# Performance work log

Measured on AMD Instinct MI355X. Metric: run time of the kernel, lower is better.

The kernel has to match this reference:

```python
import jax, jax.numpy as jnp
import numpy as np

N_NODES = 100000
D_FEAT = 128
N_EDGES = 300000
HIDDEN = 64


def setup_inputs() -> dict:
    key = jax.random.key(0)
    k1, k2, k3, k4 = jax.random.split(key, 4)
    node_emb = jax.random.normal(k1, (N_NODES, D_FEAT), dtype=jnp.float32)
    train_sample = jax.random.randint(k2, (N_EDGES, 2), 0, N_NODES, dtype=jnp.int64)
    input_dim = 2 * D_FEAT
    r1 = np.sqrt(6.0 / input_dim)
    w1 = jax.random.uniform(k3, (input_dim, HIDDEN), minval=-r1, maxval=r1, dtype=jnp.float32)
    b1 = jnp.zeros((HIDDEN,), dtype=jnp.float32)
    r2 = np.sqrt(6.0 / HIDDEN)
    w2 = jax.random.uniform(k4, (HIDDEN, 1), minval=-r2, maxval=r2, dtype=jnp.float32)
    return {"input": node_emb, "train_sample": train_sample, "w1": w1, "b1": b1, "w2": w2}


def reference(input, train_sample, w1, b1, w2):
    # gather source/target node embeddings: [E, D] each
    src = input[train_sample[:, 0]]
    dst = input[train_sample[:, 1]]
    h = jnp.concatenate([src, dst], axis=1)  # [E, 2D]
    x = jax.nn.relu(h @ w1 + b1)             # [E, HIDDEN]
    return x @ w2                             # [E, 1]
```

## Files before the change

kernel.cpp:

```cpp
#include <hip/hip_runtime.h>
#include <hip/hip_bf16.h>


#define D_FEAT 128
#define HIDDEN 64

typedef __attribute__((ext_vector_type(8))) short v8s;
typedef __attribute__((ext_vector_type(4))) float f32x4;

__device__ inline unsigned short f2bf(float f) {
    unsigned u = __builtin_bit_cast(unsigned, f);
    unsigned r = (u + 0x7FFFu + ((u >> 16) & 1u)) >> 16;
    return (unsigned short)r;
}
__device__ inline float bf2f(unsigned short u) {
    return __builtin_bit_cast(float, (unsigned)u << 16);
}

__device__ inline bool detect_is64(const int* ts32, int lane) {
    int probe = ts32[2 * lane + 1];
    return __ballot(probe != 0) == 0ULL;
}

__global__ void __launch_bounds__(256)
precompute_kernel(const float* __restrict__ emb, const float* __restrict__ w1,
                  const float* __restrict__ b1, unsigned short* __restrict__ P,
                  int n_nodes) {
    __shared__ unsigned short bt[16384];
    const int t = threadIdx.x;

    {
        const int k    = t & 127;
        const int half = t >> 7;
        const float4* src = reinterpret_cast<const float4*>(w1 + (size_t)t * 64);
#pragma unroll
        for (int j4 = 0; j4 < 16; ++j4) {
            const float4 v = src[j4];
            const int cb = half * 64 + j4 * 4;
            bt[((cb + 0) * 128 + k) ^ (((cb + 0) & 7) << 3)] = f2bf(v.x);
            bt[((cb + 1) * 128 + k) ^ (((cb + 1) & 7) << 3)] = f2bf(v.y);
            bt[((cb + 2) * 128 + k) ^ (((cb + 2) & 7) << 3)] = f2bf(v.z);
            bt[((cb + 3) * 128 + k) ^ (((cb + 3) & 7) << 3)] = f2bf(v.w);
        }
    }
    __syncthreads();

    const int lane = t & 63;
    const int wid  = t >> 6;
    const int sub  = lane & 15;
    const int g    = lane >> 4;
    const int base = blockIdx.x * 128 + wid * 32;

    const float* aptr[2];
#pragma unroll
    for (int tl = 0; tl < 2; ++tl) {
        int arow = base + tl * 16 + sub;
        if (arow >= n_nodes) arow = n_nodes - 1;
        aptr[tl] = emb + (size_t)arow * D_FEAT + g * 8;
    }

    f32x4 acc[2][8];
#pragma unroll
    for (int tl = 0; tl < 2; ++tl)
#pragma unroll
        for (int nj = 0; nj < 8; ++nj) acc[tl][nj] = (f32x4){0.f, 0.f, 0.f, 0.f};

#pragma unroll
    for (int ks = 0; ks < 4; ++ks) {
        const int k0 = ks * 32;
        v8s af[2];
#pragma unroll
        for (int tl = 0; tl < 2; ++tl) {
            const float4 a0 = *reinterpret_cast<const float4*>(aptr[tl] + k0);
            const float4 a1 = *reinterpret_cast<const float4*>(aptr[tl] + k0 + 4);
            af[tl][0] = (short)f2bf(a0.x); af[tl][1] = (short)f2bf(a0.y);
            af[tl][2] = (short)f2bf(a0.z); af[tl][3] = (short)f2bf(a0.w);
            af[tl][4] = (short)f2bf(a1.x); af[tl][5] = (short)f2bf(a1.y);
            af[tl][6] = (short)f2bf(a1.z); af[tl][7] = (short)f2bf(a1.w);
        }
#pragma unroll
        for (int nj = 0; nj < 8; ++nj) {
            const int c = nj * 16 + sub;
            const int eidx = (c * 128 + k0 + g * 8) ^ ((c & 7) << 3);
            const v8s bf = *reinterpret_cast<const v8s*>(&bt[eidx]);
            acc[0][nj] = __builtin_amdgcn_mfma_f32_16x16x32_bf16(bf, af[0], acc[0][nj], 0, 0, 0);
            acc[1][nj] = __builtin_amdgcn_mfma_f32_16x16x32_bf16(bf, af[1], acc[1][nj], 0, 0, 0);
        }
    }

    float4 bias[4];
#pragma unroll
    for (int nj = 0; nj < 4; ++nj)
        bias[nj] = *reinterpret_cast<const float4*>(b1 + nj * 16 + g * 4);

#pragma unroll
    for (int tl = 0; tl < 2; ++tl) {
        const int node = base + tl * 16 + sub;
        if (node < n_nodes) {
#pragma unroll
            for (int nj = 0; nj < 8; ++nj) {
                float b0 = 0.f, b1v = 0.f, b2 = 0.f, b3 = 0.f;
                if (nj < 4) { b0 = bias[nj].x; b1v = bias[nj].y;
                              b2 = bias[nj].z; b3 = bias[nj].w; }
                ushort4 o;
                o.x = f2bf(acc[tl][nj][0] + b0);
                o.y = f2bf(acc[tl][nj][1] + b1v);
                o.z = f2bf(acc[tl][nj][2] + b2);
                o.w = f2bf(acc[tl][nj][3] + b3);
                *reinterpret_cast<ushort4*>(P + (size_t)node * 128 + nj * 16 + g * 4) = o;
            }
        }
    }
}

__global__ void __launch_bounds__(256)
edge_kernel(const unsigned short* __restrict__ P, const void* __restrict__ ts,
            const float* __restrict__ w2, float* __restrict__ out, int n_edges) {
    const int lane = threadIdx.x & 63;
    const int wid  = threadIdx.x >> 6;
    const int sub  = lane & 15;
    const int grp  = lane >> 4;
    const int gw   = blockIdx.x * 4 + wid;
    const int nw   = gridDim.x * 4;

    const int* ts32 = (const int*)ts;
    const long long* ts64 = (const long long*)ts;
    const bool is64 = detect_is64(ts32, lane);

    const float4 w2v = *reinterpret_cast<const float4*>(w2 + sub * 4);

    for (int e = gw * 4 + grp; e < n_edges; e += nw * 4) {
        long long s, d;
        if (is64) { s = ts64[2 * e]; d = ts64[2 * e + 1]; }
        else      { s = ts32[2 * e]; d = ts32[2 * e + 1]; }
        const ushort4 a = *reinterpret_cast<const ushort4*>(P + (size_t)s * 128 + sub * 4);
        const ushort4 b = *reinterpret_cast<const ushort4*>(P + (size_t)d * 128 + 64 + sub * 4);
        float h0 = bf2f(a.x) + bf2f(b.x);
        float h1 = bf2f(a.y) + bf2f(b.y);
        float h2 = bf2f(a.z) + bf2f(b.z);
        float h3 = bf2f(a.w) + bf2f(b.w);
        h0 = h0 > 0.f ? h0 : 0.f; h1 = h1 > 0.f ? h1 : 0.f;
        h2 = h2 > 0.f ? h2 : 0.f; h3 = h3 > 0.f ? h3 : 0.f;
        float v = h0 * w2v.x + h1 * w2v.y + h2 * w2v.z + h3 * w2v.w;
#pragma unroll
        for (int off = 8; off > 0; off >>= 1) v += __shfl_xor(v, off);
        if (sub == 0) out[e] = v;
    }
}

__global__ void __launch_bounds__(256)
direct_kernel(const float* __restrict__ emb, const void* __restrict__ ts,
              const float* __restrict__ w1, const float* __restrict__ b1,
              const float* __restrict__ w2, float* __restrict__ out, int n_edges) {
    const int lane = threadIdx.x & 63;
    const int gw   = blockIdx.x * (blockDim.x >> 6) + (threadIdx.x >> 6);
    const int nw   = gridDim.x * (blockDim.x >> 6);
    const float w2v  = w2[lane];
    const float bias = b1[lane];
    const int* ts32 = (const int*)ts;
    const long long* ts64 = (const long long*)ts;
    const bool is64 = detect_is64(ts32, lane);

    for (int e = gw; e < n_edges; e += nw) {
        long long s, d;
        if (is64) { s = ts64[2 * e]; d = ts64[2 * e + 1]; }
        else      { s = ts32[2 * e]; d = ts32[2 * e + 1]; }
        const float4* s4 = reinterpret_cast<const float4*>(emb + s * D_FEAT);
        const float4* d4 = reinterpret_cast<const float4*>(emb + d * D_FEAT);
        float acc = bias;
#pragma unroll
        for (int k4 = 0; k4 < 32; ++k4) {
            float4 r = s4[k4];
            acc += r.x * w1[(4 * k4 + 0) * 64 + lane];
            acc += r.y * w1[(4 * k4 + 1) * 64 + lane];
            acc += r.z * w1[(4 * k4 + 2) * 64 + lane];
            acc += r.w * w1[(4 * k4 + 3) * 64 + lane];
        }
#pragma unroll
        for (int k4 = 0; k4 < 32; ++k4) {
            float4 r = d4[k4];
            acc += r.x * w1[(128 + 4 * k4 + 0) * 64 + lane];
            acc += r.y * w1[(128 + 4 * k4 + 1) * 64 + lane];
            acc += r.z * w1[(128 + 4 * k4 + 2) * 64 + lane];
            acc += r.w * w1[(128 + 4 * k4 + 3) * 64 + lane];
        }
        float h = acc > 0.0f ? acc : 0.0f;
        float v = h * w2v;
#pragma unroll
        for (int off = 32; off > 0; off >>= 1) v += __shfl_xor(v, off);
        if (lane == 0) out[e] = v;
    }
}

extern "C" void kernel_launch(void* const* d_in, const int* in_sizes, int n_in,
                              void* d_out, int out_size, void* d_ws, size_t ws_size,
                              hipStream_t stream) {
    const float* emb = (const float*)d_in[0];
    const void*  ts  = d_in[1];
    const float* w1  = (const float*)d_in[2];
    const float* b1  = (const float*)d_in[3];
    const float* w2  = (const float*)d_in[4];
    float* out = (float*)d_out;

    const int n_nodes = in_sizes[0] / D_FEAT;
    const int n_edges = in_sizes[1] / 2;

    const size_t p_bytes = (size_t)n_nodes * 128 * sizeof(unsigned short);

    if (ws_size >= p_bytes) {
        unsigned short* P = (unsigned short*)d_ws;
        const int nblocks = (n_nodes + 127) / 128;
        precompute_kernel<<<nblocks, 256, 0, stream>>>(emb, w1, b1, P, n_nodes);
        edge_kernel<<<2048, 256, 0, stream>>>(P, ts, w2, out, n_edges);
    } else {
        direct_kernel<<<2048, 256, 0, stream>>>(emb, ts, w1, b1, w2, out, n_edges);
    }
}
```

Before: 45.68 us.

## Shrink precompute tile, prefetch A before LDS fill, widen edge loads

The precompute kernel now gives each wave 16 nodes instead of 32 and launches twice as many blocks with a min-blocks launch bound, so the MFMA stage uses fewer registers and more blocks can be resident. The embedding rows are loaded into registers before the W1 shared-memory fill, so that global load latency overlaps the LDS writes. The edge kernel uses 8 lanes per edge with 16-byte loads instead of 16 lanes with 8-byte loads, which halves the shuffle reduction depth and doubles the edges handled per wave. The cost is that every block still stages the full W1 tile into LDS, and there are now twice as many blocks doing so.

Measured after the change: 45.89 us. No clear change (+0.5%).

```diff
diff --git a/kernel.cpp b/kernel.cpp
--- a/kernel.cpp
+++ b/kernel.cpp
@@ -22,12 +22,27 @@
     return __ballot(probe != 0) == 0ULL;
 }
 
-__global__ void __launch_bounds__(256)
+__global__ void __launch_bounds__(256, 4)
 precompute_kernel(const float* __restrict__ emb, const float* __restrict__ w1,
                   const float* __restrict__ b1, unsigned short* __restrict__ P,
                   int n_nodes) {
     __shared__ unsigned short bt[16384];
-    const int t = threadIdx.x;
+    const int t    = threadIdx.x;
+    const int lane = t & 63;
+    const int wid  = t >> 6;
+    const int sub  = lane & 15;
+    const int g    = lane >> 4;
+    const int m0   = blockIdx.x * 64 + wid * 16;
+
+    int arow = m0 + sub;
+    if (arow >= n_nodes) arow = n_nodes - 1;
+    const float* aptr = emb + (size_t)arow * D_FEAT + g * 8;
+    float4 a[8];
+#pragma unroll
+    for (int ks = 0; ks < 4; ++ks) {
+        a[2 * ks]     = *reinterpret_cast<const float4*>(aptr + ks * 32);
+        a[2 * ks + 1] = *reinterpret_cast<const float4*>(aptr + ks * 32 + 4);
+    }
 
     {
         const int k    = t & 127;
@@ -45,46 +60,25 @@
     }
     __syncthreads();
 
-    const int lane = t & 63;
-    const int wid  = t >> 6;
-    const int sub  = lane & 15;
-    const int g    = lane >> 4;
-    const int base = blockIdx.x * 128 + wid * 32;
-
-    const float* aptr[2];
-#pragma unroll
-    for (int tl = 0; tl < 2; ++tl) {
-        int arow = base + tl * 16 + sub;
-        if (arow >= n_nodes) arow = n_nodes - 1;
-        aptr[tl] = emb + (size_t)arow * D_FEAT + g * 8;
-    }
-
-    f32x4 acc[2][8];
-#pragma unroll
-    for (int tl = 0; tl < 2; ++tl)
-#pragma unroll
-        for (int nj = 0; nj < 8; ++nj) acc[tl][nj] = (f32x4){0.f, 0.f, 0.f, 0.f};
+    f32x4 acc[8];
+#pragma unroll
+    for (int nj = 0; nj < 8; ++nj) acc[nj] = (f32x4){0.f, 0.f, 0.f, 0.f};
 
 #pragma unroll
     for (int ks = 0; ks < 4; ++ks) {
         const int k0 = ks * 32;
-        v8s af[2];
-#pragma unroll
-        for (int tl = 0; tl < 2; ++tl) {
-            const float4 a0 = *reinterpret_cast<const float4*>(aptr[tl] + k0);
-            const float4 a1 = *reinterpret_cast<const float4*>(aptr[tl] + k0 + 4);
-            af[tl][0] = (short)f2bf(a0.x); af[tl][1] = (short)f2bf(a0.y);
-            af[tl][2] = (short)f2bf(a0.z); af[tl][3] = (short)f2bf(a0.w);
-            af[tl][4] = (short)f2bf(a1.x); af[tl][5] = (short)f2bf(a1.y);
-            af[tl][6] = (short)f2bf(a1.z); af[tl][7] = (short)f2bf(a1.w);
-        }
+        const float4 a0 = a[2 * ks], a1 = a[2 * ks + 1];
+        v8s af;
+        af[0] = (short)f2bf(a0.x); af[1] = (short)f2bf(a0.y);
+        af[2] = (short)f2bf(a0.z); af[3] = (short)f2bf(a0.w);
+        af[4] = (short)f2bf(a1.x); af[5] = (short)f2bf(a1.y);
+        af[6] = (short)f2bf(a1.z); af[7] = (short)f2bf(a1.w);
 #pragma unroll
         for (int nj = 0; nj < 8; ++nj) {
             const int c = nj * 16 + sub;
             const int eidx = (c * 128 + k0 + g * 8) ^ ((c & 7) << 3);
             const v8s bf = *reinterpret_cast<const v8s*>(&bt[eidx]);
-            acc[0][nj] = __builtin_amdgcn_mfma_f32_16x16x32_bf16(bf, af[0], acc[0][nj], 0, 0, 0);
-            acc[1][nj] = __builtin_amdgcn_mfma_f32_16x16x32_bf16(bf, af[1], acc[1][nj], 0, 0, 0);
+            acc[nj] = __builtin_amdgcn_mfma_f32_16x16x32_bf16(bf, af, acc[nj], 0, 0, 0);
         }
     }
 
@@ -93,24 +87,31 @@
     for (int nj = 0; nj < 4; ++nj)
         bias[nj] = *reinterpret_cast<const float4*>(b1 + nj * 16 + g * 4);
 
-#pragma unroll
-    for (int tl = 0; tl < 2; ++tl) {
-        const int node = base + tl * 16 + sub;
-        if (node < n_nodes) {
-#pragma unroll
-            for (int nj = 0; nj < 8; ++nj) {
-                float b0 = 0.f, b1v = 0.f, b2 = 0.f, b3 = 0.f;
-                if (nj < 4) { b0 = bias[nj].x; b1v = bias[nj].y;
-                              b2 = bias[nj].z; b3 = bias[nj].w; }
-                ushort4 o;
-                o.x = f2bf(acc[tl][nj][0] + b0);
-                o.y = f2bf(acc[tl][nj][1] + b1v);
-                o.z = f2bf(acc[tl][nj][2] + b2);
-                o.w = f2bf(acc[tl][nj][3] + b3);
-                *reinterpret_cast<ushort4*>(P + (size_t)node * 128 + nj * 16 + g * 4) = o;
-            }
-        }
-    }
+    const int node = m0 + sub;
+    if (node < n_nodes) {
+#pragma unroll
+        for (int nj = 0; nj < 8; ++nj) {
+            float b0 = 0.f, b1v = 0.f, b2 = 0.f, b3 = 0.f;
+            if (nj < 4) { b0 = bias[nj].x; b1v = bias[nj].y;
+                          b2 = bias[nj].z; b3 = bias[nj].w; }
+            ushort4 o;
+            o.x = f2bf(acc[nj][0] + b0);
+            o.y = f2bf(acc[nj][1] + b1v);
+            o.z = f2bf(acc[nj][2] + b2);
+            o.w = f2bf(acc[nj][3] + b3);
+            *reinterpret_cast<ushort4*>(P + (size_t)node * 128 + nj * 16 + g * 4) = o;
+        }
+    }
+}
+
+__device__ inline float pairterm(unsigned aw, unsigned bw, float w0, float w1) {
+    float a0 = __builtin_bit_cast(float, aw << 16);
+    float a1 = __builtin_bit_cast(float, aw & 0xFFFF0000u);
+    float b0 = __builtin_bit_cast(float, bw << 16);
+    float b1 = __builtin_bit_cast(float, bw & 0xFFFF0000u);
+    float h0 = a0 + b0; h0 = h0 > 0.f ? h0 : 0.f;
+    float h1 = a1 + b1; h1 = h1 > 0.f ? h1 : 0.f;
+    return h0 * w0 + h1 * w1;
 }
 
 __global__ void __launch_bounds__(256)
@@ -118,8 +119,8 @@
             const float* __restrict__ w2, float* __restrict__ out, int n_edges) {
     const int lane = threadIdx.x & 63;
     const int wid  = threadIdx.x >> 6;
-    const int sub  = lane & 15;
-    const int grp  = lane >> 4;
+    const int sub  = lane & 7;
+    const int grp  = lane >> 3;
     const int gw   = blockIdx.x * 4 + wid;
     const int nw   = gridDim.x * 4;
 
@@ -127,23 +128,21 @@
     const long long* ts64 = (const long long*)ts;
     const bool is64 = detect_is64(ts32, lane);
 
-    const float4 w2v = *reinterpret_cast<const float4*>(w2 + sub * 4);
-
-    for (int e = gw * 4 + grp; e < n_edges; e += nw * 4) {
+    const float4 w2a = *reinterpret_cast<const float4*>(w2 + sub * 8);
+    const float4 w2b = *reinterpret_cast<const float4*>(w2 + sub * 8 + 4);
+
+    for (int e = gw * 8 + grp; e < n_edges; e += nw * 8) {
         long long s, d;
         if (is64) { s = ts64[2 * e]; d = ts64[2 * e + 1]; }
         else      { s = ts32[2 * e]; d = ts32[2 * e + 1]; }
-        const ushort4 a = *reinterpret_cast<const ushort4*>(P + (size_t)s * 128 + sub * 4);
-        const ushort4 b = *reinterpret_cast<const ushort4*>(P + (size_t)d * 128 + 64 + sub * 4);
-        float h0 = bf2f(a.x) + bf2f(b.x);
-        float h1 = bf2f(a.y) + bf2f(b.y);
-        float h2 = bf2f(a.z) + bf2f(b.z);
-        float h3 = bf2f(a.w) + bf2f(b.w);
-        h0 = h0 > 0.f ? h0 : 0.f; h1 = h1 > 0.f ? h1 : 0.f;
-        h2 = h2 > 0.f ? h2 : 0.f; h3 = h3 > 0.f ? h3 : 0.f;
-        float v = h0 * w2v.x + h1 * w2v.y + h2 * w2v.z + h3 * w2v.w;
-#pragma unroll
-        for (int off = 8; off > 0; off >>= 1) v += __shfl_xor(v, off);
+        const uint4 a = *reinterpret_cast<const uint4*>(P + (size_t)s * 128 + sub * 8);
+        const uint4 b = *reinterpret_cast<const uint4*>(P + (size_t)d * 128 + 64 + sub * 8);
+        float v = pairterm(a.x, b.x, w2a.x, w2a.y)
+                + pairterm(a.y, b.y, w2a.z, w2a.w)
+                + pairterm(a.z, b.z, w2b.x, w2b.y)
+                + pairterm(a.w, b.w, w2b.z, w2b.w);
+#pragma unroll
+        for (int off = 1; off < 8; off <<= 1) v += __shfl_xor(v, off);
         if (sub == 0) out[e] = v;
     }
 }
@@ -209,7 +208,7 @@
 
     if (ws_size >= p_bytes) {
         unsigned short* P = (unsigned short*)d_ws;
-        const int nblocks = (n_nodes + 127) / 128;
+        const int nblocks = (n_nodes + 63) / 64;
         precompute_kernel<<<nblocks, 256, 0, stream>>>(emb, w1, b1, P, n_nodes);
         edge_kernel<<<2048, 256, 0, stream>>>(P, ts, w2, out, n_edges);
     } else {
```
